# Performance work log

Hardware: AMD Instinct MI355X
Metric: run time of the kernel (lower is better)

## Reference

```python
import jax, jax.numpy as jnp
import numpy as np

V, H, B, S = 128, 512, 512, 256


def setup_inputs() -> dict:
    key = jax.random.key(0)
    ks = jax.random.split(key, 12)
    s = 0.02
    inp = {
        'x': jax.random.randint(ks[0], (B, S), 0, V),
        # gate order: i, f, o, g (candidate)
        'Wx_f': jax.random.normal(ks[1], (4, H, V), jnp.float32) * s,
        'Wh_f': jax.random.normal(ks[2], (4, H, H), jnp.float32) * s,
        'bx_f': jnp.zeros((4, H), jnp.float32),
        'bh_f': jnp.zeros((4, H), jnp.float32),
        'Wx_b': jax.random.normal(ks[3], (4, H, V), jnp.float32) * s,
        'Wh_b': jax.random.normal(ks[4], (4, H, H), jnp.float32) * s,
        'bx_b': jnp.zeros((4, H), jnp.float32),
        'bh_b': jnp.zeros((4, H), jnp.float32),
        'Wfc': jax.random.normal(ks[5], (V, 2 * H), jnp.float32) * s,
        'bfc': jnp.zeros((V,), jnp.float32),
    }
    return inp


def _lstm_scan(xoh, Wx, Wh, bx, bh):
    # xoh: [S, B, V]; Wx: [4, H, V]; Wh: [4, H, H]
    b = xoh.shape[1]
    h0 = jnp.zeros((b, Wh.shape[-1]), xoh.dtype)
    c0 = jnp.zeros_like(h0)
    # precompute input contribution for all timesteps: one GEMM
    gx = jnp.einsum('sbv,ghv->sgbh', xoh, Wx) + bx[None, :, None, :]  # [S,4,B,H]

    def step(carry, gxt):
        h, c = carry
        g = gxt + jnp.einsum('bh,gkh->gbk', h, Wh) + bh[:, None, :]  # [4,B,H]
        i = jax.nn.sigmoid(g[0])
        f = jax.nn.sigmoid(g[1])
        o = jax.nn.sigmoid(g[2])
        gg = jnp.tanh(g[3])
        c = f * c + i * gg
        h = o * jnp.tanh(c)
        return (h, c), h

    _, hs = jax.lax.scan(step, (h0, c0), gx)
    return hs  # [S, B, H]


def reference(x, Wx_f, Wh_f, bx_f, bh_f, Wx_b, Wh_b, bx_b, bh_b, Wfc, bfc):
    xoh = jax.nn.one_hot(x, V, dtype=jnp.float32)           # [B,S,V]
    xoh = jnp.transpose(xoh, (1, 0, 2))                      # [S,B,V]
    hf = _lstm_scan(xoh, Wx_f, Wh_f, bx_f, bh_f)             # [S,B,H]
    hb = _lstm_scan(xoh[::-1], Wx_b, Wh_b, bx_b, bh_b)[::-1] # [S,B,H]
    comb = jnp.concatenate([hf, hb], axis=-1)                # [S,B,2H]
    y = jnp.einsum('sbh,vh->sbv', comb, Wfc) + bfc           # [S,B,V]
    return jnp.transpose(y, (1, 0, 2))                       # [B,S,V]
```

## Files before the change

### kernel.cpp

```cpp
#include <hip/hip_runtime.h>

#define Hd 512
#define Bd 512
#define Vd 128
#define Sd 256

typedef _Float16 half8 __attribute__((ext_vector_type(8)));
typedef _Float16 half4v __attribute__((ext_vector_type(4)));
typedef float float4v __attribute__((ext_vector_type(4)));
typedef unsigned int uint4v __attribute__((ext_vector_type(4)));

__device__ __forceinline__ float sigf(float v) { return 1.0f / (1.0f + __expf(-v)); }
__device__ __forceinline__ float tanhfast(float v) { return 1.0f - 2.0f / (__expf(2.0f * v) + 1.0f); }

__device__ __forceinline__ void load_lds16(const void* g, void* l) {
  __builtin_amdgcn_global_load_lds(
      (const __attribute__((address_space(1))) unsigned int*)g,
      (__attribute__((address_space(3))) unsigned int*)l, 16, 0, 0);
}

#if __has_builtin(__builtin_amdgcn_raw_buffer_load_b128) && \
    __has_builtin(__builtin_amdgcn_make_buffer_rsrc)
#define USE_BUFLD 1
#else
#define USE_BUFLD 0
#endif

#if USE_BUFLD
__device__ __forceinline__ half8 load_frag(__amdgpu_buffer_rsrc_t rs,
                                           const _Float16* base, unsigned voff) {
  uint4v d = __builtin_amdgcn_raw_buffer_load_b128(rs, voff, 0, 17 );
  union { uint4v u; half8 h; } cv; cv.u = d;
  return cv.h;
}
#else
typedef int __amdgpu_buffer_rsrc_dummy_t;
#define __amdgpu_buffer_rsrc_t __amdgpu_buffer_rsrc_dummy_t
__device__ __forceinline__ half8 load_frag(__amdgpu_buffer_rsrc_t rs,
                                           const _Float16* base, unsigned voff) {
  (void)rs;
  const char* p = (const char*)base + voff;
  union { unsigned long long u[2]; half8 h; } cv;
  cv.u[0] = __hip_atomic_load((const unsigned long long*)p, __ATOMIC_RELAXED,
                              __HIP_MEMORY_SCOPE_AGENT);
  cv.u[1] = __hip_atomic_load((const unsigned long long*)(p + 8), __ATOMIC_RELAXED,
                              __HIP_MEMORY_SCOPE_AGENT);
  return cv.h;
#endif
#if !USE_BUFLD
}
#endif

__device__ __forceinline__ void storeh4_coh(_Float16* base, unsigned voff, half4v v) {
  char* p = (char*)base + voff;
  union { unsigned long long u; half4v h; } cv;
  cv.h = v;
  __hip_atomic_store((unsigned long long*)p, cv.u, __ATOMIC_RELAXED,
                     __HIP_MEMORY_SCOPE_AGENT);
}

__global__ __launch_bounds__(256) void prep_wxt(
    const float* __restrict__ WxF, const float* __restrict__ bxF, const float* __restrict__ bhF,
    const float* __restrict__ WxB, const float* __restrict__ bxB, const float* __restrict__ bhB,
    float* __restrict__ wxt) {
  int e = blockIdx.x * 256 + threadIdx.x;
  int n = e & 2047;
  int v = (e >> 11) & 127;
  int dir = e >> 18;
  int k = n >> 2, g = n & 3;
  const float* Wx = dir ? WxB : WxF;
  const float* bx = dir ? bxB : bxF;
  const float* bh = dir ? bhB : bhF;
  int gk = g * Hd + k;
  wxt[e] = Wx[gk * Vd + v] + bx[gk] + bh[gk];
}

__global__ __launch_bounds__(256) void prep_wh16(
    const float* __restrict__ WhF, const float* __restrict__ WhB, _Float16* __restrict__ whr) {
  int e = blockIdx.x * 256 + threadIdx.x;
  int hc = e & 511;
  int n = (e >> 9) & 2047;
  int dir = e >> 20;
  int k = n >> 2, g = n & 3;
  const float* Wh = dir ? WhB : WhF;
  whr[e] = (_Float16)Wh[(g * Hd + k) * Hd + hc];
}

__global__ __launch_bounds__(256) void prep_wfc16(
    const float* __restrict__ Wfc, _Float16* __restrict__ wfc16) {
  int e = blockIdx.x * 256 + threadIdx.x;
  int hc = e & 511;
  int v = (e >> 9) & 127;
  int dir = e >> 16;
  wfc16[e] = (_Float16)Wfc[v * 1024 + dir * 512 + hc];
}

__global__ __launch_bounds__(256) void prep_xT(const int* __restrict__ x, int* __restrict__ xT) {
  int e = blockIdx.x * 256 + threadIdx.x;
  int t = e >> 9, b = e & 511;
  xT[e] = x[b * Sd + t];
}

__global__ __launch_bounds__(256) void init_zero(float* __restrict__ p) {
  int e = blockIdx.x * 256 + threadIdx.x;
  float4 z; z.x = 0.f; z.y = 0.f; z.z = 0.f; z.w = 0.f;
  ((float4*)p)[e] = z;
}

__global__ __launch_bounds__(256) void init_out(const float* __restrict__ bfc,
                                                float* __restrict__ out) {
  int e = blockIdx.x * 256 + threadIdx.x;
  int v0 = (e & 31) * 4;
  ((float4*)out)[e] = *(const float4*)&bfc[v0];
}

#define SMEM_BYTES (131072 + 17408)

#define ISSUE2(D, CC)                                                          \
  _Pragma("unroll") for (int mi = 0; mi < 2; ++mi)                             \
  _Pragma("unroll") for (int j = 0; j < 2; ++j)                                \
      D[mi][j] = load_frag(rs, hbuf, aoff[mi] + (unsigned)(((CC) * 2 + j) * 1024));

#define COMPUTE2(D, CC)                                                        \
  _Pragma("unroll") for (int j = 0; j < 2; ++j) {                              \
    const int kcabs = ks * 8 + (CC) * 2 + j;                                   \
    half8 bf[4];                                                               \
    _Pragma("unroll") for (int ni = 0; ni < 4; ++ni)                           \
        bf[ni] = *(const half8*)((const char*)smem + brow[ni] +                \
                                 (((kcabs * 4 + kq) ^ bxor[ni]) * 16));        \
    _Pragma("unroll") for (int mi = 0; mi < 2; ++mi)                           \
    _Pragma("unroll") for (int ni = 0; ni < 4; ++ni)                           \
        acc[mi][ni] = __builtin_amdgcn_mfma_f32_16x16x32_f16(                  \
            D[mi][j], bf[ni], acc[mi][ni], 0, 0, 0);                           \
  }

__global__ __launch_bounds__(512, 1) void bilstm_persist(
    const float* __restrict__ wxt, const int* __restrict__ xT,
    const _Float16* __restrict__ whr, const _Float16* __restrict__ wfc16,
    _Float16* __restrict__ hbuf, unsigned* __restrict__ flags,
    float* __restrict__ out) {
  extern __shared__ char smem[];
  _Float16* GT = (_Float16*)(smem + 131072);

  const int tid = threadIdx.x;
  const int lane = tid & 63;
  const int w = tid >> 6;
  const int ks = w >> 2;
  const int wl = w & 3;
  const int bid = blockIdx.x;
  const int grp = bid >> 4;
  const int nt = bid & 15;
  const int dir = grp >> 3;
  const int mt = grp & 7;
  const int b0 = mt * 64;

  {
    const char* wsrc = (const char*)(whr + ((size_t)(dir * 2048 + nt * 128)) * Hd);
#pragma unroll
    for (int i = 0; i < 16; ++i) {
      int e = i * 512 + tid;
      int n = e >> 6, cs = e & 63;
      load_lds16(wsrc + (size_t)n * 1024 + (size_t)(((cs ^ (n & 7)) * 16)),
                 (char*)smem + (size_t)e * 16);
    }
  }

  const int l15 = lane & 15;
  const int kq = lane >> 4;
  const int wm0 = (wl & 1) * 32;
  const int wn0 = (wl >> 1) * 64;

#if USE_BUFLD
  const __amdgpu_buffer_rsrc_t rs = __builtin_amdgcn_make_buffer_rsrc(
      (void*)hbuf, (short)0, (int)(4u * 2u * 524288u), 0x00020000);
#else
  const __amdgpu_buffer_rsrc_t rs = 0;
#endif

  const unsigned bt_base = (unsigned)((b0 >> 4) + (wl & 1) * 2);
  unsigned aoff_lane[2];
#pragma unroll
  for (int mi = 0; mi < 2; ++mi)
    aoff_lane[mi] = (bt_base + mi) * 16384u + kq * 256u + l15 * 16u +
                    (unsigned)ks * 8192u;

  int brow[4], bxor[4];
#pragma unroll
  for (int ni = 0; ni < 4; ++ni) {
    int n = wn0 + ni * 16 + l15;
    brow[ni] = n * 1024;
    bxor[ni] = n & 7;
  }

  float creg[4];
#pragma unroll
  for (int i = 0; i < 4; ++i) creg[i] = 0.f;

  const int bl = tid & 63;
  const int kh = tid >> 6;
  const int fcn = nt & 7;
  const unsigned soff_lane = (unsigned)(((b0 + bl) >> 4)) * 16384u +
                             (unsigned)(nt * 4 + (kh >> 1)) * 256u +
                             (unsigned)(bl & 15) * 16u + (unsigned)(kh & 1) * 8u;
  const unsigned fcoff_lane = (unsigned)((b0 >> 4) + wl) * 16384u + kq * 256u +
                              l15 * 16u + (unsigned)ks * 8192u;

  __syncthreads();

  for (int s = 0; s <= Sd; ++s) {
    const unsigned ph = (unsigned)(s & 3);
    const unsigned abase = (ph * 2u + (unsigned)dir) * 524288u;
    const unsigned nbase = (((unsigned)(s + 1) & 3u) * 2u + (unsigned)dir) * 524288u;

    if (s < Sd) {
      unsigned aoff[2];
      aoff[0] = abase + aoff_lane[0];
      aoff[1] = abase + aoff_lane[1];
      float4v acc[2][4];
#pragma unroll
      for (int mi = 0; mi < 2; ++mi)
#pragma unroll
        for (int ni = 0; ni < 4; ++ni) acc[mi][ni] = (float4v)0.f;

      half8 a0[2][2], a1[2][2], a2[2][2], a3[2][2];
      ISSUE2(a0, 0)
      ISSUE2(a1, 1)
      ISSUE2(a2, 2)
      COMPUTE2(a0, 0)
      ISSUE2(a3, 3)
      COMPUTE2(a1, 1)
      COMPUTE2(a2, 2)
      COMPUTE2(a3, 3)

      const int t = dir ? (Sd - 1 - s) : s;
      const int b = b0 + bl;
      const int xv = xT[t * Bd + b];
      const float* wrow = wxt + ((size_t)(dir * Vd + xv)) * 2048 + nt * 128 + kh * 16;
      float4 wv[4];
#pragma unroll
      for (int kl = 0; kl < 4; ++kl) wv[kl] = *(const float4*)&wrow[kl * 4];

      if (ks == 1) {
#pragma unroll
        for (int mi = 0; mi < 2; ++mi) {
          int m = wm0 + mi * 16 + kq * 4;
#pragma unroll
          for (int ni = 0; ni < 4; ++ni) {
            int n = wn0 + ni * 16 + l15;
            half4v hv4;
            hv4[0] = (_Float16)acc[mi][ni][0];
            hv4[1] = (_Float16)acc[mi][ni][1];
            hv4[2] = (_Float16)acc[mi][ni][2];
            hv4[3] = (_Float16)acc[mi][ni][3];
            *(half4v*)&GT[n * 68 + m] = hv4;
          }
        }
      }
      __syncthreads();
      if (ks == 0) {
#pragma unroll
        for (int mi = 0; mi < 2; ++mi) {
          int m = wm0 + mi * 16 + kq * 4;
#pragma unroll
          for (int ni = 0; ni < 4; ++ni) {
            int n = wn0 + ni * 16 + l15;
            half4v g4 = *(half4v*)&GT[n * 68 + m];
            half4v hv4;
            hv4[0] = (_Float16)(acc[mi][ni][0] + (float)g4[0]);
            hv4[1] = (_Float16)(acc[mi][ni][1] + (float)g4[1]);
            hv4[2] = (_Float16)(acc[mi][ni][2] + (float)g4[2]);
            hv4[3] = (_Float16)(acc[mi][ni][3] + (float)g4[3]);
            *(half4v*)&GT[n * 68 + m] = hv4;
          }
        }
      }
      __syncthreads();

      half4v hv;
#pragma unroll
      for (int kl = 0; kl < 4; ++kl) {
        int kloc = kh * 4 + kl;
        float g0 = (float)GT[(kloc * 4 + 0) * 68 + bl] + wv[kl].x;
        float g1 = (float)GT[(kloc * 4 + 1) * 68 + bl] + wv[kl].y;
        float g2 = (float)GT[(kloc * 4 + 2) * 68 + bl] + wv[kl].z;
        float g3 = (float)GT[(kloc * 4 + 3) * 68 + bl] + wv[kl].w;
        float gi = sigf(g0), gf = sigf(g1), go = sigf(g2), gg = tanhfast(g3);
        float cn = gf * creg[kl] + gi * gg;
        creg[kl] = cn;
        hv[kl] = (_Float16)(go * tanhfast(cn));
      }
      storeh4_coh(hbuf, nbase + soff_lane, hv);

      __syncthreads();
      if (tid == 0)
        __hip_atomic_store(&flags[bid * 32], (unsigned)(s + 1), __ATOMIC_RELAXED,
                           __HIP_MEMORY_SCOPE_AGENT);
    }

    const bool fc_act = (s & 1) ? (nt < 8) : (nt >= 8);
    if (s > 0 && fc_act) {
      const unsigned fo = abase + fcoff_lane;
      const _Float16* Bfc = wfc16 + (size_t)dir * (Vd * Hd) +
                            (size_t)(fcn * 16 + l15) * Hd + kq * 8 + ks * 256;
      half8 aF[8];
#pragma unroll
      for (int k = 0; k < 8; ++k) aF[k] = load_frag(rs, hbuf, fo + k * 1024u);
      float4v fa = (float4v)0.f;
#pragma unroll
      for (int k = 0; k < 8; ++k)
        fa = __builtin_amdgcn_mfma_f32_16x16x32_f16(aF[k], *(const half8*)(Bfc + k * 32),
                                                    fa, 0, 0, 0);
      const int tf = dir ? (Sd - s) : (s - 1);
      const int v = fcn * 16 + l15;
      const int bb = b0 + wl * 16 + kq * 4;
      float* op = out + ((size_t)bb * Sd + tf) * Vd + v;
#pragma unroll
      for (int r2 = 0; r2 < 4; ++r2)
        unsafeAtomicAdd(op + (size_t)r2 * (Sd * Vd), fa[r2]);
    }

    if (s == Sd) break;

    if (tid < 16) {
      unsigned* f = flags + (grp * 16 + tid) * 32;
      while (__hip_atomic_load(f, __ATOMIC_RELAXED, __HIP_MEMORY_SCOPE_AGENT) <
             (unsigned)(s + 1))
        __builtin_amdgcn_s_sleep(1);
    }
    __syncthreads();
  }
}

extern "C" void kernel_launch(void* const* d_in, const int* in_sizes, int n_in,
                              void* d_out, int out_size, void* d_ws, size_t ws_size,
                              hipStream_t stream) {
  (void)in_sizes; (void)n_in; (void)out_size; (void)ws_size;
  const int* x      = (const int*)d_in[0];
  const float* WxF  = (const float*)d_in[1];
  const float* WhF  = (const float*)d_in[2];
  const float* bxF  = (const float*)d_in[3];
  const float* bhF  = (const float*)d_in[4];
  const float* WxB  = (const float*)d_in[5];
  const float* WhB  = (const float*)d_in[6];
  const float* bxB  = (const float*)d_in[7];
  const float* bhB  = (const float*)d_in[8];
  const float* Wfc  = (const float*)d_in[9];
  const float* bfc  = (const float*)d_in[10];
  float* out = (float*)d_out;

  float* ws = (float*)d_ws;
  float* wxt        = ws;
  _Float16* hbuf    = (_Float16*)(ws + 524288);
  unsigned* flags   = (unsigned*)(ws + 1572864);
  _Float16* wh16    = (_Float16*)(ws + 1581056);
  _Float16* wfc16   = (_Float16*)(ws + 2629632);
  int* xT           = (int*)(ws + 2695168);

  prep_wxt<<<2048, 256, 0, stream>>>(WxF, bxF, bhF, WxB, bxB, bhB, wxt);
  prep_wh16<<<8192, 256, 0, stream>>>(WhF, WhB, wh16);
  prep_wfc16<<<512, 256, 0, stream>>>(Wfc, wfc16);
  prep_xT<<<512, 256, 0, stream>>>(x, xT);
  init_zero<<<256, 256, 0, stream>>>(ws + 524288);
  init_zero<<<8, 256, 0, stream>>>(ws + 1572864);
  init_out<<<16384, 256, 0, stream>>>(bfc, out);

  static bool attr_set = false;
  if (!attr_set) {
    (void)hipFuncSetAttribute((const void*)bilstm_persist,
                              hipFuncAttributeMaxDynamicSharedMemorySize, SMEM_BYTES);
    attr_set = true;
  }
  void* kargs[] = {(void*)&wxt, (void*)&xT, (void*)&wh16, (void*)&wfc16,
                   (void*)&hbuf, (void*)&flags, (void*)&out};
  if (hipLaunchCooperativeKernel((const void*)bilstm_persist, dim3(256), dim3(512),
                                 kargs, SMEM_BYTES, stream) != hipSuccess) {
    bilstm_persist<<<dim3(256), dim3(512), SMEM_BYTES, stream>>>(
        wxt, xT, wh16, wfc16, hbuf, flags, out);
  }
}
```

Baseline: 1.756 ms.

## Remap LSTM blocks per XCD, reshape warp tiles, reuse h fragments for FC

Each block now takes its role from a per-XCD atomic counter, so the 16 blocks sharing a batch group sit on the same XCD and their flag polling and h exchange stay in one L2. The warp tile changes from 2x4 to 1x8 MFMA tiles, so each warp loads one A row-block and reuses it across 8 B tiles. The FC projection reuses the already loaded h fragments instead of reloading them. Buffer loads drop the cache-bypass bits and h stores become plain stores. Both rely on same-XCD L2 coherence, which breaks if the counter is not reset between launches or if the XCD layout differs.

```diff
diff --git a/kernel.cpp b/kernel.cpp
--- a/kernel.cpp
+++ b/kernel.cpp
@@ -29,13 +29,12 @@
 #if USE_BUFLD
 __device__ __forceinline__ half8 load_frag(__amdgpu_buffer_rsrc_t rs,
                                            const _Float16* base, unsigned voff) {
-  uint4v d = __builtin_amdgcn_raw_buffer_load_b128(rs, voff, 0, 17 );
+  uint4v d = __builtin_amdgcn_raw_buffer_load_b128(rs, voff, 0, 1 );
   union { uint4v u; half8 h; } cv; cv.u = d;
   return cv.h;
 }
 #else
-typedef int __amdgpu_buffer_rsrc_dummy_t;
-#define __amdgpu_buffer_rsrc_t __amdgpu_buffer_rsrc_dummy_t
+typedef int __amdgpu_buffer_rsrc_t;
 __device__ __forceinline__ half8 load_frag(__amdgpu_buffer_rsrc_t rs,
                                            const _Float16* base, unsigned voff) {
   (void)rs;
@@ -46,17 +45,11 @@
   cv.u[1] = __hip_atomic_load((const unsigned long long*)(p + 8), __ATOMIC_RELAXED,
                               __HIP_MEMORY_SCOPE_AGENT);
   return cv.h;
+}
 #endif
-#if !USE_BUFLD
-}
-#endif
-
-__device__ __forceinline__ void storeh4_coh(_Float16* base, unsigned voff, half4v v) {
-  char* p = (char*)base + voff;
-  union { unsigned long long u; half4v h; } cv;
-  cv.h = v;
-  __hip_atomic_store((unsigned long long*)p, cv.u, __ATOMIC_RELAXED,
-                     __HIP_MEMORY_SCOPE_AGENT);
+
+__device__ __forceinline__ void storeh4(_Float16* base, unsigned voff, half4v v) {
+  *(half4v*)((char*)base + voff) = v;
 }
 
 __global__ __launch_bounds__(256) void prep_wxt(
@@ -116,23 +109,24 @@
 
 #define SMEM_BYTES (131072 + 17408)
 
-#define ISSUE2(D, CC)                                                          \
-  _Pragma("unroll") for (int mi = 0; mi < 2; ++mi)                             \
+#define ISSUE2(D, C)                                                           \
   _Pragma("unroll") for (int j = 0; j < 2; ++j)                                \
-      D[mi][j] = load_frag(rs, hbuf, aoff[mi] + (unsigned)(((CC) * 2 + j) * 1024));
-
-#define COMPUTE2(D, CC)                                                        \
+      D[j] = load_frag(rs, hbuf, aoff + (unsigned)(((C) * 2 + j) * 1024));
+
+#define COMPUTE2(D, C)                                                         \
   _Pragma("unroll") for (int j = 0; j < 2; ++j) {                              \
-    const int kcabs = ks * 8 + (CC) * 2 + j;                                   \
-    half8 bf[4];                                                               \
-    _Pragma("unroll") for (int ni = 0; ni < 4; ++ni)                           \
-        bf[ni] = *(const half8*)((const char*)smem + brow[ni] +                \
+    const int kcabs = ks * 8 + (C) * 2 + j;                                    \
+    _Pragma("unroll") for (int ni = 0; ni < 8; ++ni) {                         \
+      half8 bf = *(const half8*)((const char*)smem + brow[ni] +                \
                                  (((kcabs * 4 + kq) ^ bxor[ni]) * 16));        \
-    _Pragma("unroll") for (int mi = 0; mi < 2; ++mi)                           \
-    _Pragma("unroll") for (int ni = 0; ni < 4; ++ni)                           \
-        acc[mi][ni] = __builtin_amdgcn_mfma_f32_16x16x32_f16(                  \
-            D[mi][j], bf[ni], acc[mi][ni], 0, 0, 0);                           \
-  }
+      acc[ni] = __builtin_amdgcn_mfma_f32_16x16x32_f16(D[j], bf, acc[ni], 0, 0, 0); \
+    }                                                                          \
+  }
+
+#define FCC(D, C)                                                              \
+  _Pragma("unroll") for (int j = 0; j < 2; ++j)                                \
+      fa = __builtin_amdgcn_mfma_f32_16x16x32_f16(                             \
+          D[j], *(const half8*)(Bfc + ((C) * 2 + j) * 32), fa, 0, 0, 0);
 
 __global__ __launch_bounds__(512, 1) void bilstm_persist(
     const float* __restrict__ wxt, const int* __restrict__ xT,
@@ -147,12 +141,21 @@
   const int w = tid >> 6;
   const int ks = w >> 2;
   const int wl = w & 3;
-  const int bid = blockIdx.x;
-  const int grp = bid >> 4;
-  const int nt = bid & 15;
+
+  unsigned xcd;
+  asm volatile("s_getreg_b32 %0, hwreg(HW_REG_XCC_ID)" : "=s"(xcd));
+  xcd &= 7u;
+  unsigned* xcdctr = flags + 8176;
+  int* roleSh = (int*)GT;
+  if (tid == 0) roleSh[0] = (int)atomicAdd(&xcdctr[xcd], 1u);
+  __syncthreads();
+  const int rank = roleSh[0];
+  const int grp = (int)xcd * 2 + (rank >> 4);
+  const int nt = rank & 15;
   const int dir = grp >> 3;
   const int mt = grp & 7;
   const int b0 = mt * 64;
+  __syncthreads();
 
   {
     const char* wsrc = (const char*)(whr + ((size_t)(dir * 2048 + nt * 128)) * Hd);
@@ -167,27 +170,21 @@
 
   const int l15 = lane & 15;
   const int kq = lane >> 4;
-  const int wm0 = (wl & 1) * 32;
-  const int wn0 = (wl >> 1) * 64;
 
 #if USE_BUFLD
   const __amdgpu_buffer_rsrc_t rs = __builtin_amdgcn_make_buffer_rsrc(
-      (void*)hbuf, (short)0, (int)(4u * 2u * 524288u), 0x00020000);
+      (void*)hbuf, (short)0, (int)4194304, 0x00020000);
 #else
   const __amdgpu_buffer_rsrc_t rs = 0;
 #endif
 
-  const unsigned bt_base = (unsigned)((b0 >> 4) + (wl & 1) * 2);
-  unsigned aoff_lane[2];
-#pragma unroll
-  for (int mi = 0; mi < 2; ++mi)
-    aoff_lane[mi] = (bt_base + mi) * 16384u + kq * 256u + l15 * 16u +
-                    (unsigned)ks * 8192u;
-
-  int brow[4], bxor[4];
-#pragma unroll
-  for (int ni = 0; ni < 4; ++ni) {
-    int n = wn0 + ni * 16 + l15;
+  const unsigned aoff_lane = (unsigned)((b0 >> 4) + wl) * 16384u + kq * 256u +
+                             l15 * 16u + (unsigned)ks * 8192u;
+
+  int brow[8], bxor[8];
+#pragma unroll
+  for (int ni = 0; ni < 8; ++ni) {
+    int n = ni * 16 + l15;
     brow[ni] = n * 1024;
     bxor[ni] = n & 7;
   }
@@ -199,30 +196,25 @@
   const int bl = tid & 63;
   const int kh = tid >> 6;
   const int fcn = nt & 7;
+  const int gtm = wl * 16 + kq * 4;
   const unsigned soff_lane = (unsigned)(((b0 + bl) >> 4)) * 16384u +
                              (unsigned)(nt * 4 + (kh >> 1)) * 256u +
                              (unsigned)(bl & 15) * 16u + (unsigned)(kh & 1) * 8u;
-  const unsigned fcoff_lane = (unsigned)((b0 >> 4) + wl) * 16384u + kq * 256u +
-                              l15 * 16u + (unsigned)ks * 8192u;
 
   __syncthreads();
 
   for (int s = 0; s <= Sd; ++s) {
-    const unsigned ph = (unsigned)(s & 3);
-    const unsigned abase = (ph * 2u + (unsigned)dir) * 524288u;
+    const unsigned abase = (((unsigned)(s & 3)) * 2u + (unsigned)dir) * 524288u;
     const unsigned nbase = (((unsigned)(s + 1) & 3u) * 2u + (unsigned)dir) * 524288u;
+    const unsigned aoff = abase + aoff_lane;
+
+    half8 a0[2], a1[2], a2[2], a3[2];
 
     if (s < Sd) {
-      unsigned aoff[2];
-      aoff[0] = abase + aoff_lane[0];
-      aoff[1] = abase + aoff_lane[1];
-      float4v acc[2][4];
-#pragma unroll
-      for (int mi = 0; mi < 2; ++mi)
-#pragma unroll
-        for (int ni = 0; ni < 4; ++ni) acc[mi][ni] = (float4v)0.f;
-
-      half8 a0[2][2], a1[2][2], a2[2][2], a3[2][2];
+      float4v acc[8];
+#pragma unroll
+      for (int ni = 0; ni < 8; ++ni) acc[ni] = (float4v)0.f;
+
       ISSUE2(a0, 0)
       ISSUE2(a1, 1)
       ISSUE2(a2, 2)
@@ -242,36 +234,28 @@
 
       if (ks == 1) {
 #pragma unroll
-        for (int mi = 0; mi < 2; ++mi) {
-          int m = wm0 + mi * 16 + kq * 4;
-#pragma unroll
-          for (int ni = 0; ni < 4; ++ni) {
-            int n = wn0 + ni * 16 + l15;
-            half4v hv4;
-            hv4[0] = (_Float16)acc[mi][ni][0];
-            hv4[1] = (_Float16)acc[mi][ni][1];
-            hv4[2] = (_Float16)acc[mi][ni][2];
-            hv4[3] = (_Float16)acc[mi][ni][3];
-            *(half4v*)&GT[n * 68 + m] = hv4;
-          }
+        for (int ni = 0; ni < 8; ++ni) {
+          int n = ni * 16 + l15;
+          half4v hv4;
+          hv4[0] = (_Float16)acc[ni][0];
+          hv4[1] = (_Float16)acc[ni][1];
+          hv4[2] = (_Float16)acc[ni][2];
+          hv4[3] = (_Float16)acc[ni][3];
+          *(half4v*)&GT[n * 68 + gtm] = hv4;
         }
       }
       __syncthreads();
       if (ks == 0) {
 #pragma unroll
-        for (int mi = 0; mi < 2; ++mi) {
-          int m = wm0 + mi * 16 + kq * 4;
-#pragma unroll
-          for (int ni = 0; ni < 4; ++ni) {
-            int n = wn0 + ni * 16 + l15;
-            half4v g4 = *(half4v*)&GT[n * 68 + m];
-            half4v hv4;
-            hv4[0] = (_Float16)(acc[mi][ni][0] + (float)g4[0]);
-            hv4[1] = (_Float16)(acc[mi][ni][1] + (float)g4[1]);
-            hv4[2] = (_Float16)(acc[mi][ni][2] + (float)g4[2]);
-            hv4[3] = (_Float16)(acc[mi][ni][3] + (float)g4[3]);
-            *(half4v*)&GT[n * 68 + m] = hv4;
-          }
+        for (int ni = 0; ni < 8; ++ni) {
+          int n = ni * 16 + l15;
+          half4v g4 = *(half4v*)&GT[n * 68 + gtm];
+          half4v hv4;
+          hv4[0] = (_Float16)(acc[ni][0] + (float)g4[0]);
+          hv4[1] = (_Float16)(acc[ni][1] + (float)g4[1]);
+          hv4[2] = (_Float16)(acc[ni][2] + (float)g4[2]);
+          hv4[3] = (_Float16)(acc[ni][3] + (float)g4[3]);
+          *(half4v*)&GT[n * 68 + gtm] = hv4;
         }
       }
       __syncthreads();
@@ -289,27 +273,28 @@
         creg[kl] = cn;
         hv[kl] = (_Float16)(go * tanhfast(cn));
       }
-      storeh4_coh(hbuf, nbase + soff_lane, hv);
+      storeh4(hbuf, nbase + soff_lane, hv);
 
       __syncthreads();
       if (tid == 0)
-        __hip_atomic_store(&flags[bid * 32], (unsigned)(s + 1), __ATOMIC_RELAXED,
-                           __HIP_MEMORY_SCOPE_AGENT);
+        __hip_atomic_store(&flags[(grp * 16 + nt) * 32], (unsigned)(s + 1),
+                           __ATOMIC_RELAXED, __HIP_MEMORY_SCOPE_AGENT);
+    } else {
+      ISSUE2(a0, 0)
+      ISSUE2(a1, 1)
+      ISSUE2(a2, 2)
+      ISSUE2(a3, 3)
     }
 
     const bool fc_act = (s & 1) ? (nt < 8) : (nt >= 8);
     if (s > 0 && fc_act) {
-      const unsigned fo = abase + fcoff_lane;
       const _Float16* Bfc = wfc16 + (size_t)dir * (Vd * Hd) +
-                            (size_t)(fcn * 16 + l15) * Hd + kq * 8 + ks * 256;
-      half8 aF[8];
-#pragma unroll
-      for (int k = 0; k < 8; ++k) aF[k] = load_frag(rs, hbuf, fo + k * 1024u);
+                            (size_t)(fcn * 16 + l15) * Hd + ks * 256 + kq * 8;
       float4v fa = (float4v)0.f;
-#pragma unroll
-      for (int k = 0; k < 8; ++k)
-        fa = __builtin_amdgcn_mfma_f32_16x16x32_f16(aF[k], *(const half8*)(Bfc + k * 32),
-                                                    fa, 0, 0, 0);
+      FCC(a0, 0)
+      FCC(a1, 1)
+      FCC(a2, 2)
+      FCC(a3, 3)
       const int tf = dir ? (Sd - s) : (s - 1);
       const int v = fcn * 16 + l15;
       const int bb = b0 + wl * 16 + kq * 4;
```

New measurement: 1.614 ms. 8.1% less time.
